# Optimization experiments

Measured on AMD Instinct MI355X. Metric: run time of the kernel, lower is better.

The kernel has to match this reference:

```python
import jax, jax.numpy as jnp
import numpy as np

MIN_DEPTH = 0.001  # validity threshold used by the torch module


def setup_inputs() -> dict:
    key = jax.random.key(0)
    k1, k2 = jax.random.split(key)
    B, P, H, W = 8, 256, 240, 320
    # bin edges in a plausible depth range [0, 10)
    bins = jax.random.uniform(k1, (B, P + 1), dtype=jnp.float32) * 10.0
    # depth maps in [0.5, 10.0): every pixel passes the ge(0.001) mask,
    # so the padded ragged path in torch equals using all pixels directly
    target_depth_maps = jax.random.uniform(k2, (B, 1, H, W), dtype=jnp.float32) * 9.5 + 0.5
    return {"bins": bins, "target_depth_maps": target_depth_maps}


def reference(bins, target_depth_maps):
    # bin centers: [B, P]
    bin_centers = 0.5 * (bins[:, 1:] + bins[:, :-1])
    B = target_depth_maps.shape[0]
    targets = target_depth_maps.reshape(B, -1)  # [B, M]
    # invalid pixels become 0.0, matching pad_sequence's zero padding value
    targets = jnp.where(targets >= MIN_DEPTH, targets, 0.0)
    # One-directional Chamfer in 1D: for each bin center, min |c - t| over
    # target points. Instead of materializing the [B, P, M] pairwise tensor
    # (as the torch code does), sort targets and use nearest-neighbor search
    # -- identical math, O(M log M) instead of O(P*M) memory traffic.
    ts = jnp.sort(targets, axis=1)  # [B, M]
    M = ts.shape[1]

    def nearest(c, t):  # c: [P] queries, t: [M] sorted targets
        idx = jnp.searchsorted(t, c)
        lo = t[jnp.clip(idx - 1, 0, M - 1)]
        hi = t[jnp.clip(idx, 0, M - 1)]
        return jnp.minimum(jnp.abs(c - lo), jnp.abs(c - hi))

    d = jax.vmap(nearest)(bin_centers, ts)  # [B, P] min distances
    return jnp.sum(d)
```

## Files before the change

### kernel.cpp

```cpp
#include <hip/hip_runtime.h>

#define NB     8
#define NP     256
#define MPB    76800
#define SLICES 128
#define PER    (MPB / SLICES)

#define MIN_DEPTH 0.001f

__global__ __launch_bounds__(256) void chamfer_min_kernel(
    const float* __restrict__ bins,
    const float* __restrict__ targets,
    unsigned int* __restrict__ minbits) {
    const int b   = blockIdx.y;
    const int s   = blockIdx.x;
    const int tid = threadIdx.x;

    __shared__ float sh[PER];

    const float4* src = reinterpret_cast<const float4*>(targets + (size_t)b * MPB + (size_t)s * PER);
    for (int i = tid; i < PER / 4; i += 256) {
        float4 t = src[i];
        t.x = (t.x >= MIN_DEPTH) ? t.x : 0.0f;
        t.y = (t.y >= MIN_DEPTH) ? t.y : 0.0f;
        t.z = (t.z >= MIN_DEPTH) ? t.z : 0.0f;
        t.w = (t.w >= MIN_DEPTH) ? t.w : 0.0f;
        reinterpret_cast<float4*>(sh)[i] = t;
    }
    __syncthreads();

    const float c = 0.5f * (bins[b * (NP + 1) + tid] + bins[b * (NP + 1) + tid + 1]);

    float m0 = 1e30f, m1 = 1e30f, m2 = 1e30f, m3 = 1e30f;
    for (int i = 0; i < PER / 4; ++i) {
        float4 t = reinterpret_cast<const float4*>(sh)[i];
        m0 = fminf(m0, fabsf(c - t.x));
        m1 = fminf(m1, fabsf(c - t.y));
        m2 = fminf(m2, fabsf(c - t.z));
        m3 = fminf(m3, fabsf(c - t.w));
    }
    float m = fminf(fminf(m0, m1), fminf(m2, m3));
    atomicMin(&minbits[b * NP + tid], __float_as_uint(m));
}

__global__ __launch_bounds__(256) void chamfer_sum_kernel(
    const unsigned int* __restrict__ minbits,
    float* __restrict__ out) {
    const int tid = threadIdx.x;
    float s = 0.0f;
    for (int i = tid; i < NB * NP; i += 256)
        s += __uint_as_float(minbits[i]);
    for (int off = 32; off > 0; off >>= 1)
        s += __shfl_down(s, off, 64);
    __shared__ float ws[4];
    if ((tid & 63) == 0) ws[tid >> 6] = s;
    __syncthreads();
    if (tid == 0) out[0] = ws[0] + ws[1] + ws[2] + ws[3];
}

extern "C" void kernel_launch(void* const* d_in, const int* in_sizes, int n_in,
                              void* d_out, int out_size, void* d_ws, size_t ws_size,
                              hipStream_t stream) {
    const float* bins    = (const float*)d_in[0];
    const float* targets = (const float*)d_in[1];
    float* out           = (float*)d_out;
    unsigned int* minbits = (unsigned int*)d_ws;

    hipMemsetAsync(minbits, 0xFF, (size_t)NB * NP * sizeof(unsigned int), stream);

    dim3 grid(SLICES, NB);
    chamfer_min_kernel<<<grid, 256, 0, stream>>>(bins, targets, minbits);
    chamfer_sum_kernel<<<1, 256, 0, stream>>>(minbits, out);
}
```

Baseline: 66.73 us.

## Register-block two centers per thread, drop LDS staging and atomics

Result: slower. 95.28 us (+42.8%).

```diff
diff --git a/kernel.cpp b/kernel.cpp
--- a/kernel.cpp
+++ b/kernel.cpp
@@ -8,54 +8,68 @@
 
 #define MIN_DEPTH 0.001f
 
-__global__ __launch_bounds__(256) void chamfer_min_kernel(
+__global__ __launch_bounds__(128) void chamfer_stage1(
     const float* __restrict__ bins,
     const float* __restrict__ targets,
-    unsigned int* __restrict__ minbits) {
+    float* __restrict__ partial) {
     const int b   = blockIdx.y;
     const int s   = blockIdx.x;
     const int tid = threadIdx.x;
 
-    __shared__ float sh[PER];
+    const float c0 = 0.5f * (bins[b * (NP + 1) + tid]       + bins[b * (NP + 1) + tid + 1]);
+    const float c1 = 0.5f * (bins[b * (NP + 1) + tid + 128] + bins[b * (NP + 1) + tid + 129]);
 
-    const float4* src = reinterpret_cast<const float4*>(targets + (size_t)b * MPB + (size_t)s * PER);
-    for (int i = tid; i < PER / 4; i += 256) {
+    const float4* src = reinterpret_cast<const float4*>(
+        targets + (size_t)b * MPB + (size_t)s * PER);
+
+    float a00 = 1e30f, a01 = 1e30f, a10 = 1e30f, a11 = 1e30f;
+#pragma unroll 5
+    for (int i = 0; i < PER / 4; ++i) {
         float4 t = src[i];
         t.x = (t.x >= MIN_DEPTH) ? t.x : 0.0f;
         t.y = (t.y >= MIN_DEPTH) ? t.y : 0.0f;
         t.z = (t.z >= MIN_DEPTH) ? t.z : 0.0f;
         t.w = (t.w >= MIN_DEPTH) ? t.w : 0.0f;
-        reinterpret_cast<float4*>(sh)[i] = t;
+        a00 = fminf(a00, fminf(fabsf(c0 - t.x), fabsf(c0 - t.y)));
+        a01 = fminf(a01, fminf(fabsf(c0 - t.z), fabsf(c0 - t.w)));
+        a10 = fminf(a10, fminf(fabsf(c1 - t.x), fabsf(c1 - t.y)));
+        a11 = fminf(a11, fminf(fabsf(c1 - t.z), fabsf(c1 - t.w)));
     }
-    __syncthreads();
 
-    const float c = 0.5f * (bins[b * (NP + 1) + tid] + bins[b * (NP + 1) + tid + 1]);
-
-    float m0 = 1e30f, m1 = 1e30f, m2 = 1e30f, m3 = 1e30f;
-    for (int i = 0; i < PER / 4; ++i) {
-        float4 t = reinterpret_cast<const float4*>(sh)[i];
-        m0 = fminf(m0, fabsf(c - t.x));
-        m1 = fminf(m1, fabsf(c - t.y));
-        m2 = fminf(m2, fabsf(c - t.z));
-        m3 = fminf(m3, fabsf(c - t.w));
-    }
-    float m = fminf(fminf(m0, m1), fminf(m2, m3));
-    atomicMin(&minbits[b * NP + tid], __float_as_uint(m));
+    float* dst = partial + ((size_t)b * SLICES + s) * NP;
+    dst[tid]       = fminf(a00, a01);
+    dst[tid + 128] = fminf(a10, a11);
 }
 
-__global__ __launch_bounds__(256) void chamfer_sum_kernel(
-    const unsigned int* __restrict__ minbits,
+__global__ __launch_bounds__(256) void chamfer_stage2(
+    const float* __restrict__ partial,
+    float* __restrict__ sums) {
+    const int b = blockIdx.x;
+    const int p = threadIdx.x;
+
+    const float* base = partial + (size_t)b * SLICES * NP + p;
+    float m = 1e30f;
+#pragma unroll 8
+    for (int s = 0; s < SLICES; ++s)
+        m = fminf(m, base[(size_t)s * NP]);
+
+    float v = m;
+    for (int off = 32; off > 0; off >>= 1)
+        v += __shfl_down(v, off, 64);
+    __shared__ float w[4];
+    if ((p & 63) == 0) w[p >> 6] = v;
+    __syncthreads();
+    if (p == 0) sums[b] = w[0] + w[1] + w[2] + w[3];
+}
+
+__global__ __launch_bounds__(64) void chamfer_stage3(
+    const float* __restrict__ sums,
     float* __restrict__ out) {
-    const int tid = threadIdx.x;
-    float s = 0.0f;
-    for (int i = tid; i < NB * NP; i += 256)
-        s += __uint_as_float(minbits[i]);
-    for (int off = 32; off > 0; off >>= 1)
-        s += __shfl_down(s, off, 64);
-    __shared__ float ws[4];
-    if ((tid & 63) == 0) ws[tid >> 6] = s;
-    __syncthreads();
-    if (tid == 0) out[0] = ws[0] + ws[1] + ws[2] + ws[3];
+    if (threadIdx.x == 0) {
+        float s = 0.0f;
+        for (int b = 0; b < NB; ++b) s += sums[b];
+        out[0] = s;
+    }
 }
 
 extern "C" void kernel_launch(void* const* d_in, const int* in_sizes, int n_in,
@@ -64,11 +78,12 @@
     const float* bins    = (const float*)d_in[0];
     const float* targets = (const float*)d_in[1];
     float* out           = (float*)d_out;
-    unsigned int* minbits = (unsigned int*)d_ws;
 
-    hipMemsetAsync(minbits, 0xFF, (size_t)NB * NP * sizeof(unsigned int), stream);
+    float* partial = (float*)d_ws;
+    float* sums    = partial + (size_t)NB * SLICES * NP;
 
-    dim3 grid(SLICES, NB);
-    chamfer_min_kernel<<<grid, 256, 0, stream>>>(bins, targets, minbits);
-    chamfer_sum_kernel<<<1, 256, 0, stream>>>(minbits, out);
+    dim3 grid1(SLICES, NB);
+    chamfer_stage1<<<grid1, 128, 0, stream>>>(bins, targets, partial);
+    chamfer_stage2<<<NB, 256, 0, stream>>>(partial, sums);
+    chamfer_stage3<<<1, 64, 0, stream>>>(sums, out);
 }
```
